# Kernel tuning notes

Measured on AMD Instinct MI355X. Metric: run time of the kernel, lower is better.

Reference implementation:

```python
import jax, jax.numpy as jnp
import numpy as np

B, T, C_IN, H, NC = 256, 512, 64, 256, 6


def setup_inputs() -> dict:
    key = jax.random.key(0)
    ks = jax.random.split(key, 12)
    s = 0.05  # init scale for stability
    return {
        "x":    jax.random.normal(ks[0], (B, T, C_IN), dtype=jnp.float32),
        "Wih0": jax.random.normal(ks[1], (4 * H, C_IN), dtype=jnp.float32) * s,
        "Whh0": jax.random.normal(ks[2], (4 * H, H), dtype=jnp.float32) * s,
        "bih0": jax.random.normal(ks[3], (4 * H,), dtype=jnp.float32) * s,
        "bhh0": jax.random.normal(ks[4], (4 * H,), dtype=jnp.float32) * s,
        "Wih1": jax.random.normal(ks[5], (4 * H, H), dtype=jnp.float32) * s,
        "Whh1": jax.random.normal(ks[6], (4 * H, H), dtype=jnp.float32) * s,
        "bih1": jax.random.normal(ks[7], (4 * H,), dtype=jnp.float32) * s,
        "bhh1": jax.random.normal(ks[8], (4 * H,), dtype=jnp.float32) * s,
        "Wfc":  jax.random.normal(ks[9], (NC, H), dtype=jnp.float32) * s,
        "bfc":  jax.random.normal(ks[10], (NC,), dtype=jnp.float32) * s,
    }


def _lstm_layer(x, Wih, Whh, bih, bhh):
    # x: [B, T, D] batch_first. PyTorch/DPLSTM gate order: i, f, g, o.
    Bb, Tt, _ = x.shape
    Hh = Whh.shape[1]
    # Precompute input projections for all timesteps (one big GEMM): [T, B, 4H]
    xg = jnp.einsum('btd,gd->tbg', x, Wih) + (bih + bhh)

    def step(carry, xg_t):
        h, c = carry
        gates = xg_t + h @ Whh.T  # [B, 4H]
        i, f, g, o = jnp.split(gates, 4, axis=-1)
        i = jax.nn.sigmoid(i)
        f = jax.nn.sigmoid(f)
        g = jnp.tanh(g)
        o = jax.nn.sigmoid(o)
        c = f * c + i * g
        h = o * jnp.tanh(c)
        return (h, c), h

    h0 = jnp.zeros((Bb, Hh), dtype=x.dtype)
    c0 = jnp.zeros((Bb, Hh), dtype=x.dtype)
    _, hs = jax.lax.scan(step, (h0, c0), xg)  # hs: [T, B, H]
    return jnp.swapaxes(hs, 0, 1)  # [B, T, H]


def reference(x, Wih0, Whh0, bih0, bhh0, Wih1, Whh1, bih1, bhh1, Wfc, bfc):
    # 2-layer DPLSTM (inter-layer dropout p=0.0 -> identity, eval mode)
    h1 = _lstm_layer(x, Wih0, Whh0, bih0, bhh0)
    h2 = _lstm_layer(h1, Wih1, Whh1, bih1, bhh1)
    # Dropout(p=0.0) -> identity; Linear over all timesteps, then last step
    out = h2 @ Wfc.T + bfc           # [B, T, NC]
    logits = out[:, -1, :]           # [B, NC]
    return jax.nn.softmax(logits, axis=1)
```

## Files before the change

### kernel.cpp

```cpp
#include <hip/hip_runtime.h>
#include <stdint.h>

#define B_   256
#define T_   512
#define CIN  64
#define H_   256
#define G4   1024
#define NC   6

#define MB   32
#define NHU  16
#define NBG  (B_/MB)
#define NHG  (H_/NHU)
#define NWG  (NBG*NHG)

typedef __bf16 bf16x8 __attribute__((ext_vector_type(8)));
typedef __bf16 bf16x4 __attribute__((ext_vector_type(4)));
typedef float  f32x4  __attribute__((ext_vector_type(4)));

#define OFF_XBF   ((size_t)0)
#define SZ_XBF    ((size_t)B_*T_*CIN*2)
#define OFF_W0X   (OFF_XBF + SZ_XBF)
#define SZ_W0X    ((size_t)G4*CIN*2)
#define OFF_W0H   (OFF_W0X + SZ_W0X)
#define SZ_WH     ((size_t)G4*H_*2)
#define OFF_W1X   (OFF_W0H + SZ_WH)
#define OFF_W1H   (OFF_W1X + SZ_WH)
#define OFF_B0    (OFF_W1H + SZ_WH)
#define OFF_B1    (OFF_B0 + 4096)
#define OFF_APUB  (OFF_B1 + 4096)
#define SZ_PUB    ((size_t)2*B_*H_*2)
#define OFF_BPUB  (OFF_APUB + SZ_PUB)
#define OFF_SYNC  (OFF_BPUB + SZ_PUB)
#define SYNC_WORDS 512

#define DYN_LDS_ELEMS (4096 + 3*16384)
#define DYN_LDS_BYTES (DYN_LDS_ELEMS*2)

__device__ __forceinline__ f32x4 MFMA(bf16x8 a, bf16x8 b, f32x4 c) {
  return __builtin_amdgcn_mfma_f32_16x16x32_bf16(a, b, c, 0, 0, 0);
}
__device__ __forceinline__ float fsig(float x) { return 1.f/(1.f + __expf(-x)); }
__device__ __forceinline__ float ftanh_(float x) {
  float xx = fminf(fmaxf(x, -15.f), 15.f);
  float t = __expf(2.f*xx);
  return (t-1.f)/(t+1.f);
}

__device__ __forceinline__ void load8_c(const __bf16* b, bf16x8 (&r)[8]) {
  const __bf16 *p0=b,      *p1=b+32,  *p2=b+64,  *p3=b+96,
               *p4=b+128,  *p5=b+160, *p6=b+192, *p7=b+224;
  asm volatile(
    "global_load_dwordx4 %0, %8, off sc0 sc1\n\t"
    "global_load_dwordx4 %1, %9, off sc0 sc1\n\t"
    "global_load_dwordx4 %2, %10, off sc0 sc1\n\t"
    "global_load_dwordx4 %3, %11, off sc0 sc1\n\t"
    "global_load_dwordx4 %4, %12, off sc0 sc1\n\t"
    "global_load_dwordx4 %5, %13, off sc0 sc1\n\t"
    "global_load_dwordx4 %6, %14, off sc0 sc1\n\t"
    "global_load_dwordx4 %7, %15, off sc0 sc1"
    : "=&v"(r[0]), "=&v"(r[1]), "=&v"(r[2]), "=&v"(r[3]),
      "=&v"(r[4]), "=&v"(r[5]), "=&v"(r[6]), "=&v"(r[7])
    : "v"(p0), "v"(p1), "v"(p2), "v"(p3), "v"(p4), "v"(p5), "v"(p6), "v"(p7)
    : "memory");
}
__device__ __forceinline__ void waitv0() { asm volatile("s_waitcnt vmcnt(0)" ::: "memory"); }
__device__ __forceinline__ void sbar0()  { __builtin_amdgcn_sched_barrier(0); }

__device__ __forceinline__ void poll16(const unsigned* fb, unsigned tgt) {
  const unsigned* p = fb + (threadIdx.x & 15);
  for (;;) {
    unsigned v;
    asm volatile("global_load_dword %0, %1, off sc0 sc1\n\ts_waitcnt vmcnt(0)"
                 : "=&v"(v) : "v"(p) : "memory");
    if (__ballot(v >= tgt) == ~0ull) return;
    __builtin_amdgcn_s_sleep(1);
  }
}
__device__ __forceinline__ void store_stamp(unsigned* p, unsigned v) {
  asm volatile("global_store_dword %0, %1, off sc0 sc1" :: "v"(p), "v"(v) : "memory");
}
__device__ __forceinline__ void store_h16(__bf16* p, float v) {
  __bf16 h = (__bf16)v;
  unsigned u = (unsigned)__builtin_bit_cast(unsigned short, h);
  asm volatile("global_store_short %0, %1, off sc0 sc1" :: "v"(p), "v"(u) : "memory");
}

__global__ void k_prep_x(const float* __restrict__ x, __bf16* __restrict__ xbf) {
  int i = blockIdx.x * blockDim.x + threadIdx.x;
  const int n4 = (B_*T_*CIN)/4;
  if (i >= n4) return;
  float4 v = reinterpret_cast<const float4*>(x)[i];
  bf16x4 o;
  o[0] = (__bf16)v.x; o[1] = (__bf16)v.y; o[2] = (__bf16)v.z; o[3] = (__bf16)v.w;
  reinterpret_cast<bf16x4*>(xbf)[i] = o;
}

__global__ void k_prep_w(const float* __restrict__ Wih0, const float* __restrict__ Whh0,
                         const float* __restrict__ Wih1, const float* __restrict__ Whh1,
                         __bf16* __restrict__ w0x, __bf16* __restrict__ w0h,
                         __bf16* __restrict__ w1x, __bf16* __restrict__ w1h) {
  int e = blockIdx.x * blockDim.x + threadIdx.x;
  const int E0 = G4*CIN, E1 = G4*H_;
  const float* W; __bf16* dst; int K; int idx;
  if      (e < E0)        { W = Wih0; dst = w0x; K = CIN; idx = e; }
  else if (e < E0+E1)     { W = Whh0; dst = w0h; K = H_;  idx = e - E0; }
  else if (e < E0+2*E1)   { W = Wih1; dst = w1x; K = H_;  idx = e - E0 - E1; }
  else if (e < E0+3*E1)   { W = Whh1; dst = w1h; K = H_;  idx = e - E0 - 2*E1; }
  else return;
  const int kb = K >> 5;
  int j   = idx & 7;
  int cl  = (idx >> 3) & 15;
  int sb  = (idx >> 7) & 3;
  int ks  = (idx >> 9) % kb;
  int ct  = (idx / (512*kb)) & 3;
  int hj  =  idx / (2048*kb);
  int g  = ct*256 + hj*16 + cl;
  int kk = ks*32 + sb*8 + j;
  dst[idx] = (__bf16)W[(size_t)g*K + kk];
}

__global__ void k_prep_misc(const float* __restrict__ bih0, const float* __restrict__ bhh0,
                            const float* __restrict__ bih1, const float* __restrict__ bhh1,
                            float* __restrict__ bias0, float* __restrict__ bias1,
                            unsigned* __restrict__ zpub, unsigned* __restrict__ syncw) {
  int i = blockIdx.x * blockDim.x + threadIdx.x;
  if (i < G4) bias0[i] = bih0[i] + bhh0[i];
  else if (i < 2*G4) { int j = i - G4; bias1[j] = bih1[j] + bhh1[j]; }
  const int PW = (int)((2*SZ_PUB)/4);
  int zi = i - 2*G4;
  if (zi >= 0 && zi < PW) zpub[zi] = 0u;
  if (i < SYNC_WORDS) syncw[i] = 0u;
}

__global__ void __launch_bounds__(256, 1) k_lstm(
    const __bf16* __restrict__ xbf,
    const __bf16* __restrict__ w0x_g, const __bf16* __restrict__ w0h_g,
    const __bf16* __restrict__ w1x_g, const __bf16* __restrict__ w1h_g,
    const float* __restrict__ bias0, const float* __restrict__ bias1,
    __bf16* __restrict__ apub, __bf16* __restrict__ bpub,
    unsigned* __restrict__ sync,
    const float* __restrict__ Wfc, const float* __restrict__ bfc,
    float* __restrict__ out)
{
  extern __shared__ __bf16 lds[];
  __bf16* l0x = lds;
  __bf16* l0h = lds + 4096;
  __bf16* l1x = lds + 20480;
  __bf16* l1h = lds + 36864;
  __shared__ float s_log[MB][NC];

  const int tid   = threadIdx.x;
  const int bid   = blockIdx.x;
  const int bg    = bid & 7;
  const int hj    = bid >> 3;
  const int wave  = tid >> 6;
  const int lane  = tid & 63;
  const int layer = wave >> 1;
  const int mt    = wave & 1;
  const int col   = lane & 15;
  const int sub   = lane >> 4;
  const int brow  = bg*MB + mt*16;

  unsigned* stline = sync + (size_t)bg*64;
  unsigned* myst   = stline + hj;

  {
    const uint4* s; uint4* d;
    s = (const uint4*)(w0x_g + (size_t)hj*4096);  d = (uint4*)l0x;
    for (int i = tid; i < 512;  i += 256) d[i] = s[i];
    s = (const uint4*)(w0h_g + (size_t)hj*16384); d = (uint4*)l0h;
    for (int i = tid; i < 2048; i += 256) d[i] = s[i];
    s = (const uint4*)(w1x_g + (size_t)hj*16384); d = (uint4*)l1x;
    for (int i = tid; i < 2048; i += 256) d[i] = s[i];
    s = (const uint4*)(w1h_g + (size_t)hj*16384); d = (uint4*)l1h;
    for (int i = tid; i < 2048; i += 256) d[i] = s[i];
  }
  __syncthreads();

  float bs0, bs1, bs2, bs3;
  {
    const float* bp = layer ? bias1 : bias0;
    bs0 = bp[0*256 + hj*16 + col];
    bs1 = bp[1*256 + hj*16 + col];
    bs2 = bp[2*256 + hj*16 + col];
    bs3 = bp[3*256 + hj*16 + col];
  }
  float cst[4] = {0.f, 0.f, 0.f, 0.f};

  for (int k = 0; k <= T_; ++k) {
    const __bf16* a_prev = apub + (size_t)((k+1)&1)*(B_*H_);
    const __bf16* b_prev = bpub + (size_t)((k+1)&1)*(B_*H_);
    __bf16* a_cur = apub + (size_t)(k&1)*(B_*H_);
    __bf16* b_cur = bpub + (size_t)(k&1)*(B_*H_);
    const bool act0 = (layer == 0) && (k < T_);
    const bool act1 = (layer == 1) && (k >= 1);
    f32x4 acc0 = {0,0,0,0}, acc1 = {0,0,0,0}, acc2 = {0,0,0,0}, acc3 = {0,0,0,0};

    if (act0) {
      const __bf16* xr = xbf + ((size_t)(brow+col)*T_ + k)*CIN + sub*8;
      const __bf16* wb = l0x + sub*128 + col*8;
#pragma unroll
      for (int ks = 0; ks < 2; ++ks) {
        bf16x8 a = *(const bf16x8*)(xr + ks*32);
        acc0 = MFMA(a, *(const bf16x8*)(wb + ks*512 +    0), acc0);
        acc1 = MFMA(a, *(const bf16x8*)(wb + ks*512 + 1024), acc1);
        acc2 = MFMA(a, *(const bf16x8*)(wb + ks*512 + 2048), acc2);
        acc3 = MFMA(a, *(const bf16x8*)(wb + ks*512 + 3072), acc3);
      }
    }

    if (k > 0) {
      if (tid < 64) poll16(stline, (unsigned)k);
      __syncthreads();
    }

    if (act0) {
      bf16x8 ra[8];
      load8_c(a_prev + (size_t)(brow+col)*H_ + sub*8, ra);
      waitv0(); sbar0();
      const __bf16* wb = l0h + sub*128 + col*8;
#pragma unroll
      for (int ks = 0; ks < 8; ++ks) {
        acc0 = MFMA(ra[ks], *(const bf16x8*)(wb + ks*512 +     0), acc0);
        acc1 = MFMA(ra[ks], *(const bf16x8*)(wb + ks*512 +  4096), acc1);
        acc2 = MFMA(ra[ks], *(const bf16x8*)(wb + ks*512 +  8192), acc2);
        acc3 = MFMA(ra[ks], *(const bf16x8*)(wb + ks*512 + 12288), acc3);
      }
    } else if (act1) {
      bf16x8 ra[8], rb[8];
      load8_c(a_prev + (size_t)(brow+col)*H_ + sub*8, ra);
      load8_c(b_prev + (size_t)(brow+col)*H_ + sub*8, rb);
      waitv0(); sbar0();
      const __bf16* w1 = l1x + sub*128 + col*8;
      const __bf16* w2 = l1h + sub*128 + col*8;
#pragma unroll
      for (int ks = 0; ks < 8; ++ks) {
        acc0 = MFMA(ra[ks], *(const bf16x8*)(w1 + ks*512 +     0), acc0);
        acc1 = MFMA(ra[ks], *(const bf16x8*)(w1 + ks*512 +  4096), acc1);
        acc2 = MFMA(ra[ks], *(const bf16x8*)(w1 + ks*512 +  8192), acc2);
        acc3 = MFMA(ra[ks], *(const bf16x8*)(w1 + ks*512 + 12288), acc3);
      }
#pragma unroll
      for (int ks = 0; ks < 8; ++ks) {
        acc0 = MFMA(rb[ks], *(const bf16x8*)(w2 + ks*512 +     0), acc0);
        acc1 = MFMA(rb[ks], *(const bf16x8*)(w2 + ks*512 +  4096), acc1);
        acc2 = MFMA(rb[ks], *(const bf16x8*)(w2 + ks*512 +  8192), acc2);
        acc3 = MFMA(rb[ks], *(const bf16x8*)(w2 + ks*512 + 12288), acc3);
      }
    }

    if (act0 || act1) {
      __bf16* dst  = act0 ? a_cur : b_cur;
      __bf16* drow = dst + (size_t)(brow + sub*4)*H_ + hj*NHU + col;
#pragma unroll
      for (int q = 0; q < 4; ++q) {
        float gi = acc0[q] + bs0;
        float gf = acc1[q] + bs1;
        float gg = acc2[q] + bs2;
        float go = acc3[q] + bs3;
        float si = fsig(gi), sf = fsig(gf), sg = ftanh_(gg), so = fsig(go);
        float c = sf*cst[q] + si*sg;
        cst[q] = c;
        store_h16(drow + (size_t)q*H_, so * ftanh_(c));
      }
    }

    waitv0();
    __syncthreads();
    if (tid == 0) store_stamp(myst, (unsigned)(k + 1));
  }

  if (hj == 0) {
    if (tid < 64) poll16(stline, (unsigned)(T_ + 1));
    __syncthreads();
    if (tid < MB*NC) {
      int r = tid / NC, cl = tid % NC;
      const __bf16* hr = bpub + (size_t)(bg*MB + r)*H_;
      const float*  wr = Wfc + (size_t)cl*H_;
      float s = bfc[cl];
      for (int c8 = 0; c8 < 32; ++c8) {
        bf16x8 v;
        const __bf16* p = hr + c8*8;
        asm volatile("global_load_dwordx4 %0, %1, off sc0 sc1\n\ts_waitcnt vmcnt(0)"
                     : "=&v"(v) : "v"(p) : "memory");
#pragma unroll
        for (int j = 0; j < 8; ++j) s = fmaf((float)v[j], wr[c8*8+j], s);
      }
      s_log[r][cl] = s;
    }
    __syncthreads();
    if (tid < MB) {
      float mx = s_log[tid][0];
#pragma unroll
      for (int c2 = 1; c2 < NC; ++c2) mx = fmaxf(mx, s_log[tid][c2]);
      float e[NC]; float se = 0.f;
#pragma unroll
      for (int c2 = 0; c2 < NC; ++c2) { e[c2] = __expf(s_log[tid][c2] - mx); se += e[c2]; }
      float inv = 1.f/se;
#pragma unroll
      for (int c2 = 0; c2 < NC; ++c2) out[(size_t)(bg*MB + tid)*NC + c2] = e[c2]*inv;
    }
  }
}

extern "C" void kernel_launch(void* const* d_in, const int* in_sizes, int n_in,
                              void* d_out, int out_size, void* d_ws, size_t ws_size,
                              hipStream_t stream) {
  const float* x    = (const float*)d_in[0];
  const float* Wih0 = (const float*)d_in[1];
  const float* Whh0 = (const float*)d_in[2];
  const float* bih0 = (const float*)d_in[3];
  const float* bhh0 = (const float*)d_in[4];
  const float* Wih1 = (const float*)d_in[5];
  const float* Whh1 = (const float*)d_in[6];
  const float* bih1 = (const float*)d_in[7];
  const float* bhh1 = (const float*)d_in[8];
  const float* Wfc  = (const float*)d_in[9];
  const float* bfc  = (const float*)d_in[10];
  float* out = (float*)d_out;
  char*  ws  = (char*)d_ws;

  __bf16* xbf  = (__bf16*)(ws + OFF_XBF);
  __bf16* w0x  = (__bf16*)(ws + OFF_W0X);
  __bf16* w0h  = (__bf16*)(ws + OFF_W0H);
  __bf16* w1x  = (__bf16*)(ws + OFF_W1X);
  __bf16* w1h  = (__bf16*)(ws + OFF_W1H);
  float*  b0   = (float*) (ws + OFF_B0);
  float*  b1   = (float*) (ws + OFF_B1);
  __bf16* apub = (__bf16*)(ws + OFF_APUB);
  __bf16* bpub = (__bf16*)(ws + OFF_BPUB);
  unsigned* syncw = (unsigned*)(ws + OFF_SYNC);

  {
    const int n4 = (B_*T_*CIN)/4;
    k_prep_x<<<(n4 + 255)/256, 256, 0, stream>>>(x, xbf);
  }
  {
    const int tot = G4*CIN + 3*G4*H_;
    k_prep_w<<<(tot + 255)/256, 256, 0, stream>>>(Wih0, Whh0, Wih1, Whh1, w0x, w0h, w1x, w1h);
  }
  {
    const int tot = 2*G4 + (int)((2*SZ_PUB)/4);
    k_prep_misc<<<(tot + 255)/256, 256, 0, stream>>>(bih0, bhh0, bih1, bhh1, b0, b1,
                                                     (unsigned*)apub, syncw);
  }
  (void)hipFuncSetAttribute((const void*)k_lstm,
                            hipFuncAttributeMaxDynamicSharedMemorySize, DYN_LDS_BYTES);
  k_lstm<<<NWG, 256, DYN_LDS_BYTES, stream>>>(xbf, w0x, w0h, w1x, w1h, b0, b1,
                                              apub, bpub, syncw, Wfc, bfc, out);
}
```

Before: 2.609 ms.

## Share layer-0 hidden state via LDS, vectorize publish stores, and replace end barrier with counter

```diff
diff --git a/kernel.cpp b/kernel.cpp
--- a/kernel.cpp
+++ b/kernel.cpp
@@ -17,6 +17,7 @@
 typedef __bf16 bf16x8 __attribute__((ext_vector_type(8)));
 typedef __bf16 bf16x4 __attribute__((ext_vector_type(4)));
 typedef float  f32x4  __attribute__((ext_vector_type(4)));
+typedef unsigned u32x4 __attribute__((ext_vector_type(4)));
 
 #define OFF_XBF   ((size_t)0)
 #define SZ_XBF    ((size_t)B_*T_*CIN*2)
@@ -34,7 +35,8 @@
 #define OFF_SYNC  (OFF_BPUB + SZ_PUB)
 #define SYNC_WORDS 512
 
-#define DYN_LDS_ELEMS (4096 + 3*16384)
+#define AST_OFF   53248
+#define DYN_LDS_ELEMS (53248 + 8448)
 #define DYN_LDS_BYTES (DYN_LDS_ELEMS*2)
 
 __device__ __forceinline__ f32x4 MFMA(bf16x8 a, bf16x8 b, f32x4 c) {
@@ -80,10 +82,8 @@
 __device__ __forceinline__ void store_stamp(unsigned* p, unsigned v) {
   asm volatile("global_store_dword %0, %1, off sc0 sc1" :: "v"(p), "v"(v) : "memory");
 }
-__device__ __forceinline__ void store_h16(__bf16* p, float v) {
-  __bf16 h = (__bf16)v;
-  unsigned u = (unsigned)__builtin_bit_cast(unsigned short, h);
-  asm volatile("global_store_short %0, %1, off sc0 sc1" :: "v"(p), "v"(u) : "memory");
+__device__ __forceinline__ void st16_pub(__bf16* p, u32x4 v) {
+  asm volatile("global_store_dwordx4 %0, %1, off sc0 sc1" :: "v"(p), "v"(v) : "memory");
 }
 
 __global__ void k_prep_x(const float* __restrict__ x, __bf16* __restrict__ xbf) {
@@ -148,7 +148,10 @@
   __bf16* l0h = lds + 4096;
   __bf16* l1x = lds + 20480;
   __bf16* l1h = lds + 36864;
+  __bf16* ast = lds + AST_OFF;
   __shared__ float s_log[MB][NC];
+  __shared__ __align__(16) __bf16 s_stage[4][16][24];
+  __shared__ unsigned s_cnt;
 
   const int tid   = threadIdx.x;
   const int bid   = blockIdx.x;
@@ -165,6 +168,8 @@
   unsigned* stline = sync + (size_t)bg*64;
   unsigned* myst   = stline + hj;
 
+  if (tid == 0) s_cnt = 0u;
+
   {
     const uint4* s; uint4* d;
     s = (const uint4*)(w0x_g + (size_t)hj*4096);  d = (uint4*)l0x;
@@ -188,6 +193,8 @@
   }
   float cst[4] = {0.f, 0.f, 0.f, 0.f};
 
+  __bf16* amy = ast + (size_t)mt*(16*264) + (size_t)col*264;
+
   for (int k = 0; k <= T_; ++k) {
     const __bf16* a_prev = apub + (size_t)((k+1)&1)*(B_*H_);
     const __bf16* b_prev = bpub + (size_t)((k+1)&1)*(B_*H_);
@@ -215,10 +222,20 @@
       __syncthreads();
     }
 
-    if (act0) {
-      bf16x8 ra[8];
+    bf16x8 ra[8], rb[8];
+    if (layer == 0) {
       load8_c(a_prev + (size_t)(brow+col)*H_ + sub*8, ra);
       waitv0(); sbar0();
+#pragma unroll
+      for (int ks = 0; ks < 8; ++ks)
+        *reinterpret_cast<bf16x8*>(amy + ks*32 + sub*8) = ra[ks];
+    } else if (act1) {
+      load8_c(b_prev + (size_t)(brow+col)*H_ + sub*8, rb);
+    }
+
+    __syncthreads();
+
+    if (act0) {
       const __bf16* wb = l0h + sub*128 + col*8;
 #pragma unroll
       for (int ks = 0; ks < 8; ++ks) {
@@ -228,18 +245,15 @@
         acc3 = MFMA(ra[ks], *(const bf16x8*)(wb + ks*512 + 12288), acc3);
       }
     } else if (act1) {
-      bf16x8 ra[8], rb[8];
-      load8_c(a_prev + (size_t)(brow+col)*H_ + sub*8, ra);
-      load8_c(b_prev + (size_t)(brow+col)*H_ + sub*8, rb);
-      waitv0(); sbar0();
       const __bf16* w1 = l1x + sub*128 + col*8;
       const __bf16* w2 = l1h + sub*128 + col*8;
 #pragma unroll
       for (int ks = 0; ks < 8; ++ks) {
-        acc0 = MFMA(ra[ks], *(const bf16x8*)(w1 + ks*512 +     0), acc0);
-        acc1 = MFMA(ra[ks], *(const bf16x8*)(w1 + ks*512 +  4096), acc1);
-        acc2 = MFMA(ra[ks], *(const bf16x8*)(w1 + ks*512 +  8192), acc2);
-        acc3 = MFMA(ra[ks], *(const bf16x8*)(w1 + ks*512 + 12288), acc3);
+        bf16x8 ar = *reinterpret_cast<const bf16x8*>(amy + ks*32 + sub*8);
+        acc0 = MFMA(ar, *(const bf16x8*)(w1 + ks*512 +     0), acc0);
+        acc1 = MFMA(ar, *(const bf16x8*)(w1 + ks*512 +  4096), acc1);
+        acc2 = MFMA(ar, *(const bf16x8*)(w1 + ks*512 +  8192), acc2);
+        acc3 = MFMA(ar, *(const bf16x8*)(w1 + ks*512 + 12288), acc3);
       }
 #pragma unroll
       for (int ks = 0; ks < 8; ++ks) {
@@ -251,8 +265,7 @@
     }
 
     if (act0 || act1) {
-      __bf16* dst  = act0 ? a_cur : b_cur;
-      __bf16* drow = dst + (size_t)(brow + sub*4)*H_ + hj*NHU + col;
+      __bf16* dst = act0 ? a_cur : b_cur;
 #pragma unroll
       for (int q = 0; q < 4; ++q) {
         float gi = acc0[q] + bs0;
@@ -262,13 +275,23 @@
         float si = fsig(gi), sf = fsig(gf), sg = ftanh_(gg), so = fsig(go);
         float c = sf*cst[q] + si*sg;
         cst[q] = c;
-        store_h16(drow + (size_t)q*H_, so * ftanh_(c));
+        s_stage[wave][sub*4+q][col] = (__bf16)(so * ftanh_(c));
+      }
+      asm volatile("s_waitcnt lgkmcnt(0)" ::: "memory");
+      sbar0();
+      if (lane < 32) {
+        const int r16 = lane >> 1, half = lane & 1;
+        u32x4 packed = *reinterpret_cast<const u32x4*>(&s_stage[wave][r16][half*8]);
+        __bf16* pa = dst + (size_t)(bg*MB + mt*16 + r16)*H_ + hj*16 + half*8;
+        st16_pub(pa, packed);
       }
     }
 
     waitv0();
-    __syncthreads();
-    if (tid == 0) store_stamp(myst, (unsigned)(k + 1));
+    if (lane == 0) {
+      unsigned old = atomicAdd(&s_cnt, 1u);
+      if (old == 4u*(unsigned)k + 3u) store_stamp(myst, (unsigned)(k + 1));
+    }
   }
 
   if (hj == 0) {
```

Measured after the change: 5.099 ms. 95.4% more time.
